# Optimization experiments

Hardware: AMD Instinct MI355X
Metric: run time of the kernel (lower is better)

Reference implementation:

```python
import jax, jax.numpy as jnp
import numpy as np

SEQ, BATCH, INPUT, HIDDEN, OUTPUT = 4096, 512, 8, 30, 1


def setup_inputs() -> dict:
    key = jax.random.key(0)
    ks = jax.random.split(key, 8)
    s = 1.0 / np.sqrt(HIDDEN)  # torch LSTM/Linear init scale
    u = lambda k, shape: jax.random.uniform(k, shape, jnp.float32, -s, s)
    return {
        "x": jax.random.normal(ks[0], (SEQ, BATCH, INPUT), jnp.float32),
        "W_ih": u(ks[1], (4 * HIDDEN, INPUT)),   # gate order: i, f, g, o
        "W_hh": u(ks[2], (4 * HIDDEN, HIDDEN)),
        "b_ih": u(ks[3], (4 * HIDDEN,)),
        "b_hh": u(ks[4], (4 * HIDDEN,)),
        "W_lin": u(ks[5], (OUTPUT, HIDDEN)),
        "b_lin": u(ks[6], (OUTPUT,)),
    }


def _lstm(x, W_ih, W_hh, b_ih, b_hh):
    H = W_hh.shape[1]
    B = x.shape[1]
    # Precompute input projections for all timesteps: [S,B,4H]
    x_proj = jnp.einsum("sbi,gi->sbg", x, W_ih) + b_ih + b_hh

    def step(carry, xp_t):
        h, c = carry
        gates = xp_t + h @ W_hh.T  # [B,4H]
        i, f, g, o = jnp.split(gates, 4, axis=-1)
        i, f, o = jax.nn.sigmoid(i), jax.nn.sigmoid(f), jax.nn.sigmoid(o)
        c = f * c + i * jnp.tanh(g)
        h = o * jnp.tanh(c)
        return (h, c), h

    h0 = jnp.zeros((B, H), x.dtype)
    c0 = jnp.zeros((B, H), x.dtype)
    _, pred = jax.lax.scan(step, (h0, c0), x_proj)
    return pred  # [S,B,H]


def reference(x, W_ih, W_hh, b_ih, b_hh, W_lin, b_lin):
    pred = _lstm(x, W_ih, W_hh, b_ih, b_hh)
    # per-timestep Linear (loop in the original == one batched matmul)
    out = jnp.einsum("sbh,oh->sbo", pred, W_lin) + b_lin
    return out
```

## Files before the change

kernel.cpp:

```cpp
#include <hip/hip_runtime.h>

#define SEQ 4096
#define BATCH 512
#define INP 8
#define HID 30
#define LOG2E 1.44269504088896340736f

typedef float f32x2 __attribute__((ext_vector_type(2)));
typedef float f32x4 __attribute__((ext_vector_type(4)));
typedef unsigned uint2v __attribute__((ext_vector_type(2)));

#define RCP(v)  __builtin_amdgcn_rcpf(v)
#if __has_builtin(__builtin_amdgcn_exp2f)
#define EXP2(v) __builtin_amdgcn_exp2f(v)
#else
#define EXP2(v) exp2f(v)
#endif
#define PKFMA(a, b, c) __builtin_elementwise_fma(a, b, c)

__device__ __forceinline__ f32x2 mk2(float a, float b) {
    f32x2 r; r.x = a; r.y = b; return r;
}

__device__ __forceinline__ void rep_halves(float v, float& lo_rep, float& hi_rep) {
#if __has_builtin(__builtin_amdgcn_permlane32_swap)
    uint2v r = __builtin_amdgcn_permlane32_swap(
        __float_as_uint(v), __float_as_uint(v), false, false);
    lo_rep = __uint_as_float(r.x);
    hi_rep = __uint_as_float(r.y);
#else
    float other = __shfl_xor(v, 32, 64);
    bool hi = (threadIdx.x & 32) != 0;
    lo_rep = hi ? other : v;
    hi_rep = hi ? v : other;
#endif
}

template <int CTRL>
__device__ __forceinline__ float dpp_sum_step(float v) {
    return v + __uint_as_float(__builtin_amdgcn_update_dpp(
        0, (int)__float_as_uint(v), CTRL, 0xf, 0xf, true));
}

__device__ __forceinline__ float group32_reduce(float v) {
    v = dpp_sum_step<0x111>(v);
    v = dpp_sum_step<0x112>(v);
    v = dpp_sum_step<0x114>(v);
    v = dpp_sum_step<0x118>(v);
#if __has_builtin(__builtin_amdgcn_permlane16_swap)
    uint2v r = __builtin_amdgcn_permlane16_swap(
        __float_as_uint(v), __float_as_uint(v), false, false);
    return __uint_as_float(r.x) + __uint_as_float(r.y);
#else
    return v + __shfl_xor(v, 16, 64);
#endif
}

__global__ __launch_bounds__(64)
__attribute__((amdgpu_waves_per_eu(1, 1)))
void lstm_chain_kernel(
    const float* __restrict__ x,
    const float* __restrict__ W_ih,
    const float* __restrict__ W_hh,
    const float* __restrict__ b_ih,
    const float* __restrict__ b_hh,
    const float* __restrict__ W_lin,
    const float* __restrict__ b_lin,
    float* __restrict__ out)
{
    const int lane = threadIdx.x;
    const int g    = blockIdx.x;
    const int b    = (g & 7) * (BATCH / 8) + (g >> 3);
    const int j    = lane & 31;
    const int half = lane >> 5;
    const int jc   = j < HID ? j : HID - 1;
    const int ra   = half * HID + jc;
    const int rb   = 2 * HID + half * HID + jc;

    const float sA   = -LOG2E;
    const float sB   = half ? -LOG2E : 2.0f * LOG2E;
    const float T2L  = 2.0f * LOG2E;
    const float IT2L = 1.0f / (2.0f * LOG2E);
    const float sclB2 = half ? T2L : -2.0f * T2L;
    const float addB2 = half ? 0.0f : T2L;

    f32x2 wih2_a[INP / 2], wih2_b[INP / 2];
#pragma unroll
    for (int i = 0; i < INP / 2; ++i) {
        f32x2 wa = mk2(W_ih[ra * INP + 2 * i] * sA, W_ih[ra * INP + 2 * i + 1] * sA);
        f32x2 wb = mk2(W_ih[rb * INP + 2 * i] * sB, W_ih[rb * INP + 2 * i + 1] * sB);
        asm volatile("" : "+v"(wa));
        asm volatile("" : "+v"(wb));
        wih2_a[i] = wa;
        wih2_b[i] = wb;
    }
    f32x2 whh2_a[HID / 2], whh2_b[HID / 2];
#pragma unroll
    for (int k = 0; k < HID / 2; ++k) {
        f32x2 wa = mk2(W_hh[ra * HID + 2 * k] * sA, W_hh[ra * HID + 2 * k + 1] * sA);
        f32x2 wb = mk2(W_hh[rb * HID + 2 * k] * sB, W_hh[rb * HID + 2 * k + 1] * sB);
        asm volatile("" : "+v"(wa));
        asm volatile("" : "+v"(wb));
        whh2_a[k] = wa;
        whh2_b[k] = wb;
    }
    const float bias_sa = (b_ih[ra] + b_hh[ra]) * sA;
    const float bias_sb = (b_ih[rb] + b_hh[rb]) * sB;
    const float blin    = b_lin[0];
    const float wlin    = (j < HID) ? W_lin[j] : 0.0f;

    __shared__ float s_y[SEQ];
    __shared__ __align__(16) float s_x[2 * 64 * INP];

    f32x4* sx4 = reinterpret_cast<f32x4*>(s_x);
    const f32x4* sx4c = reinterpret_cast<const f32x4*>(s_x);

    float hs[HID];
#pragma unroll
    for (int k = 0; k < HID; ++k) hs[k] = 0.0f;
    float c2 = 0.0f;

    f32x4 stg0, stg1;

#define STAGELOAD(CH2) do {                                                   \
    int _b0 = (CH2) * 64 + (lane >> 1);                                       \
    int _b1 = _b0 + 32;                                                       \
    if (_b0 > SEQ - 1) _b0 = SEQ - 1;                                         \
    if (_b1 > SEQ - 1) _b1 = SEQ - 1;                                         \
    const f32x4* _p0 = (const f32x4*)(x + ((size_t)_b0 * BATCH + b) * INP) + (lane & 1); \
    const f32x4* _p1 = (const f32x4*)(x + ((size_t)_b1 * BATCH + b) * INP) + (lane & 1); \
    stg0 = *_p0;                                                              \
    stg1 = *_p1;                                                              \
} while (0)

#define STAGEWRITE(CHW) do {                                                  \
    f32x4* _d = sx4 + ((CHW) & 1) * 128;                                      \
    _d[lane]      = stg0;                                                     \
    _d[64 + lane] = stg1;                                                     \
} while (0)

#define LOADXL(XA, XB, TL) do {                                               \
    int _e = (((TL) >> 6) & 1) * 128 + ((TL) & 63) * 2;                       \
    XA = sx4c[_e];                                                            \
    XB = sx4c[_e + 1];                                                        \
} while (0)

    f32x2 preA0, preA1, preB0, preB1;

#define IHPRE(XA, XB) do {                                                    \
    f32x2 x01 = __builtin_shufflevector(XA, XA, 0, 1);                        \
    f32x2 x23 = __builtin_shufflevector(XA, XA, 2, 3);                        \
    f32x2 x45 = __builtin_shufflevector(XB, XB, 0, 1);                        \
    f32x2 x67 = __builtin_shufflevector(XB, XB, 2, 3);                        \
    preA0 = mk2(bias_sa, 0.0f);  preB0 = mk2(bias_sb, 0.0f);                  \
    preA1 = mk2(0.0f, 0.0f);     preB1 = mk2(0.0f, 0.0f);                     \
    preA0 = PKFMA(x01, wih2_a[0], preA0);  preB0 = PKFMA(x01, wih2_b[0], preB0); \
    preA1 = PKFMA(x23, wih2_a[1], preA1);  preB1 = PKFMA(x23, wih2_b[1], preB1); \
    preA0 = PKFMA(x45, wih2_a[2], preA0);  preB0 = PKFMA(x45, wih2_b[2], preB0); \
    preA1 = PKFMA(x67, wih2_a[3], preA1);  preB1 = PKFMA(x67, wih2_b[3], preB1); \
} while (0)

    STAGELOAD(0);
    STAGEWRITE(0);
    STAGELOAD(1);

    f32x4 xA0, xB0, xA1, xB1, xA2, xB2, xA3, xB3;
    LOADXL(xA0, xB0, 0);  LOADXL(xA1, xB1, 1);
    LOADXL(xA2, xB2, 2);  LOADXL(xA3, xB3, 3);
    IHPRE(xA0, xB0);

#define STEP(T, XAn, XBn, XAl, XBl, TL) do {                                  \
    f32x2 A0 = preA0, A1 = preA1, B0 = preB0, B1 = preB1;                     \
    _Pragma("unroll")                                                         \
    for (int k = 0; k < HID / 2 - 1; k += 2) {                                \
        f32x2 h0 = mk2(hs[2*k],   hs[2*k+1]);                                 \
        f32x2 h1 = mk2(hs[2*k+2], hs[2*k+3]);                                 \
        A0 = PKFMA(h0, whh2_a[k],   A0);                                      \
        B0 = PKFMA(h0, whh2_b[k],   B0);                                      \
        A1 = PKFMA(h1, whh2_a[k+1], A1);                                      \
        B1 = PKFMA(h1, whh2_b[k+1], B1);                                      \
    }                                                                         \
    {                                                                         \
        f32x2 hT = mk2(hs[HID-2], hs[HID-1]);                                 \
        A0 = PKFMA(hT, whh2_a[HID/2-1], A0);                                  \
        B0 = PKFMA(hT, whh2_b[HID/2-1], B0);                                  \
    }                                                                         \
    f32x2 As = A0 + A1;  float ua = As.x + As.y;                              \
    f32x2 Bs = B0 + B1;  float ub = Bs.x + Bs.y;                              \
    float Av  = RCP(1.0f + EXP2(ua));              \
    float sBv = RCP(1.0f + EXP2(ub));                                         \
    float Bv2 = fmaf(sBv, sclB2, addB2);   \
               \
    float m = Av * (half ? c2 : Bv2);                                         \
    float mlo, mhi;                                                           \
    rep_halves(m, mlo, mhi);                                                  \
    c2 = mlo + mhi;                                   \
    float glo, oT2;                                                           \
    rep_halves(Bv2, glo, oT2);            \
    float oo_u = oT2 * IT2L;                                                  \
    float n2o  = oT2 * (-2.0f * IT2L);                                        \
    float sc = RCP(1.0f + EXP2(c2));                                          \
    float h  = fmaf(sc, n2o, oo_u);                        \
    _Pragma("unroll")                                                         \
    for (int k = 0; k < HID; ++k)                                             \
        hs[k] = __uint_as_float((unsigned)__builtin_amdgcn_readlane(          \
                    (int)__float_as_uint(h), k));                             \
                              \
    float p = group32_reduce(h * wlin);                                       \
    if (lane == 31) s_y[T] = p + blin;                                        \
    LOADXL(XAl, XBl, TL);                                                     \
    IHPRE(XAn, XBn);                                                          \
} while (0)

    for (int ch = 0; ch < SEQ / 64; ++ch) {
        STAGEWRITE(ch + 1);
        STAGELOAD(ch + 2);
        const int t0 = ch * 64;
#pragma unroll 1
        for (int tt = 0; tt < 64; tt += 4) {
            const int t = t0 + tt;
            STEP(t + 0, xA1, xB1, xA0, xB0, t + 4);
            STEP(t + 1, xA2, xB2, xA1, xB1, t + 5);
            STEP(t + 2, xA3, xB3, xA2, xB2, t + 6);
            STEP(t + 3, xA0, xB0, xA3, xB3, t + 7);
        }
    }
#undef STEP
#undef IHPRE
#undef LOADXL
#undef STAGELOAD
#undef STAGEWRITE

    __syncthreads();
    const float4* s_y4 = reinterpret_cast<const float4*>(s_y);
#pragma unroll 4
    for (int it = 0; it < SEQ / 256; ++it) {
        int tbase = it * 256 + lane * 4;
        float4 v = s_y4[tbase >> 2];
        out[(size_t)(tbase + 0) * BATCH + b] = v.x;
        out[(size_t)(tbase + 1) * BATCH + b] = v.y;
        out[(size_t)(tbase + 2) * BATCH + b] = v.z;
        out[(size_t)(tbase + 3) * BATCH + b] = v.w;
    }
}

extern "C" void kernel_launch(void* const* d_in, const int* in_sizes, int n_in,
                              void* d_out, int out_size, void* d_ws, size_t ws_size,
                              hipStream_t stream) {
    const float* x     = (const float*)d_in[0];
    const float* W_ih  = (const float*)d_in[1];
    const float* W_hh  = (const float*)d_in[2];
    const float* b_ih  = (const float*)d_in[3];
    const float* b_hh  = (const float*)d_in[4];
    const float* W_lin = (const float*)d_in[5];
    const float* b_lin = (const float*)d_in[6];
    float* out = (float*)d_out;

    lstm_chain_kernel<<<dim3(BATCH), dim3(64), 0, stream>>>(
        x, W_ih, W_hh, b_ih, b_hh, W_lin, b_lin, out);
}
```

Measured before the change: 1.020 ms.

## Process two batch chains per wave and broadcast h via LDS

Each 64-lane block now runs two independent LSTM batch chains, interleaved so their dependent FMA and transcendental sequences can hide each other's latency. The grid is halved to 256 blocks. The 30 per-step readlane broadcasts of h are replaced by one LDS store and vector LDS reads per chain. This trades half the grid's parallelism (fewer CUs busy on a 256-CU part) and more registers for better ILP within each wave. It also relies on LDS write-then-read ordering within a single wave, with no barrier.

```diff
diff --git a/kernel.cpp b/kernel.cpp
--- a/kernel.cpp
+++ b/kernel.cpp
@@ -70,7 +70,7 @@
 {
     const int lane = threadIdx.x;
     const int g    = blockIdx.x;
-    const int b    = (g & 7) * (BATCH / 8) + (g >> 3);
+    const int b0   = 2 * ((g & 7) * 32 + (g >> 3));
     const int j    = lane & 31;
     const int half = lane >> 5;
     const int jc   = j < HID ? j : HID - 1;
@@ -109,107 +109,175 @@
     const float blin    = b_lin[0];
     const float wlin    = (j < HID) ? W_lin[j] : 0.0f;
 
-    __shared__ float s_y[SEQ];
-    __shared__ __align__(16) float s_x[2 * 64 * INP];
+    __shared__ float s_y[2 * SEQ];
+    __shared__ __align__(16) float s_h[128];
+    __shared__ __align__(16) float s_x[2 * 2 * 64 * INP];
 
     f32x4* sx4 = reinterpret_cast<f32x4*>(s_x);
     const f32x4* sx4c = reinterpret_cast<const f32x4*>(s_x);
-
-    float hs[HID];
+    const f32x4* s_h4 = reinterpret_cast<const f32x4*>(s_h);
+
+    f32x2 hrf2P[HID / 2], hrf2Q[HID / 2];
 #pragma unroll
-    for (int k = 0; k < HID; ++k) hs[k] = 0.0f;
-    float c2 = 0.0f;
-
-    f32x4 stg0, stg1;
+    for (int k = 0; k < HID / 2; ++k) { hrf2P[k] = mk2(0.0f, 0.0f); hrf2Q[k] = mk2(0.0f, 0.0f); }
+    float c2P = 0.0f, c2Q = 0.0f;
+
+    f32x4 stg0, stg1, stg2, stg3;
 
 #define STAGELOAD(CH2) do {                                                   \
-    int _b0 = (CH2) * 64 + (lane >> 1);                                       \
-    int _b1 = _b0 + 32;                                                       \
-    if (_b0 > SEQ - 1) _b0 = SEQ - 1;                                         \
-    if (_b1 > SEQ - 1) _b1 = SEQ - 1;                                         \
-    const f32x4* _p0 = (const f32x4*)(x + ((size_t)_b0 * BATCH + b) * INP) + (lane & 1); \
-    const f32x4* _p1 = (const f32x4*)(x + ((size_t)_b1 * BATCH + b) * INP) + (lane & 1); \
-    stg0 = *_p0;                                                              \
-    stg1 = *_p1;                                                              \
+    int _s0 = (CH2) * 64 + (lane >> 1);                                       \
+    int _s1 = _s0 + 32;                                                       \
+    if (_s0 > SEQ - 1) _s0 = SEQ - 1;                                         \
+    if (_s1 > SEQ - 1) _s1 = SEQ - 1;                                         \
+    const f32x4* _pP0 = (const f32x4*)(x + ((size_t)_s0 * BATCH + b0) * INP) + (lane & 1);     \
+    const f32x4* _pP1 = (const f32x4*)(x + ((size_t)_s1 * BATCH + b0) * INP) + (lane & 1);     \
+    const f32x4* _pQ0 = (const f32x4*)(x + ((size_t)_s0 * BATCH + b0 + 1) * INP) + (lane & 1); \
+    const f32x4* _pQ1 = (const f32x4*)(x + ((size_t)_s1 * BATCH + b0 + 1) * INP) + (lane & 1); \
+    stg0 = *_pP0;  stg1 = *_pP1;  stg2 = *_pQ0;  stg3 = *_pQ1;                \
 } while (0)
 
 #define STAGEWRITE(CHW) do {                                                  \
-    f32x4* _d = sx4 + ((CHW) & 1) * 128;                                      \
-    _d[lane]      = stg0;                                                     \
-    _d[64 + lane] = stg1;                                                     \
-} while (0)
-
-#define LOADXL(XA, XB, TL) do {                                               \
-    int _e = (((TL) >> 6) & 1) * 128 + ((TL) & 63) * 2;                       \
-    XA = sx4c[_e];                                                            \
-    XB = sx4c[_e + 1];                                                        \
-} while (0)
-
-    f32x2 preA0, preA1, preB0, preB1;
-
-#define IHPRE(XA, XB) do {                                                    \
-    f32x2 x01 = __builtin_shufflevector(XA, XA, 0, 1);                        \
-    f32x2 x23 = __builtin_shufflevector(XA, XA, 2, 3);                        \
-    f32x2 x45 = __builtin_shufflevector(XB, XB, 0, 1);                        \
-    f32x2 x67 = __builtin_shufflevector(XB, XB, 2, 3);                        \
-    preA0 = mk2(bias_sa, 0.0f);  preB0 = mk2(bias_sb, 0.0f);                  \
-    preA1 = mk2(0.0f, 0.0f);     preB1 = mk2(0.0f, 0.0f);                     \
-    preA0 = PKFMA(x01, wih2_a[0], preA0);  preB0 = PKFMA(x01, wih2_b[0], preB0); \
-    preA1 = PKFMA(x23, wih2_a[1], preA1);  preB1 = PKFMA(x23, wih2_b[1], preB1); \
-    preA0 = PKFMA(x45, wih2_a[2], preA0);  preB0 = PKFMA(x45, wih2_b[2], preB0); \
-    preA1 = PKFMA(x67, wih2_a[3], preA1);  preB1 = PKFMA(x67, wih2_b[3], preB1); \
+    f32x4* _d = sx4 + ((CHW) & 1) * 256;                                      \
+    _d[lane]       = stg0;                                                    \
+    _d[64 + lane]  = stg1;                                                    \
+    _d[128 + lane] = stg2;                                                    \
+    _d[192 + lane] = stg3;                                                    \
+} while (0)
+
+#define LOADXL2(XAP, XBP, XAQ, XBQ, TL) do {                                  \
+    int _e = (((TL) >> 6) & 1) * 256 + ((TL) & 63) * 2;                       \
+    XAP = sx4c[_e];        XBP = sx4c[_e + 1];                                \
+    XAQ = sx4c[128 + _e];  XBQ = sx4c[128 + _e + 1];                          \
+} while (0)
+
+    f32x2 preA0P, preA1P, preB0P, preB1P;
+    f32x2 preA0Q, preA1Q, preB0Q, preB1Q;
+
+#define IHPRE2(XAP, XBP, XAQ, XBQ) do {                                       \
+    f32x2 p01 = __builtin_shufflevector(XAP, XAP, 0, 1);                      \
+    f32x2 q01 = __builtin_shufflevector(XAQ, XAQ, 0, 1);                      \
+    f32x2 p23 = __builtin_shufflevector(XAP, XAP, 2, 3);                      \
+    f32x2 q23 = __builtin_shufflevector(XAQ, XAQ, 2, 3);                      \
+    f32x2 p45 = __builtin_shufflevector(XBP, XBP, 0, 1);                      \
+    f32x2 q45 = __builtin_shufflevector(XBQ, XBQ, 0, 1);                      \
+    f32x2 p67 = __builtin_shufflevector(XBP, XBP, 2, 3);                      \
+    f32x2 q67 = __builtin_shufflevector(XBQ, XBQ, 2, 3);                      \
+    preA0P = PKFMA(p01, wih2_a[0], mk2(bias_sa, 0.0f));                       \
+    preA0Q = PKFMA(q01, wih2_a[0], mk2(bias_sa, 0.0f));                       \
+    preB0P = PKFMA(p01, wih2_b[0], mk2(bias_sb, 0.0f));                       \
+    preB0Q = PKFMA(q01, wih2_b[0], mk2(bias_sb, 0.0f));                       \
+    preA1P = PKFMA(p23, wih2_a[1], mk2(0.0f, 0.0f));                          \
+    preA1Q = PKFMA(q23, wih2_a[1], mk2(0.0f, 0.0f));                          \
+    preB1P = PKFMA(p23, wih2_b[1], mk2(0.0f, 0.0f));                          \
+    preB1Q = PKFMA(q23, wih2_b[1], mk2(0.0f, 0.0f));                          \
+    preA0P = PKFMA(p45, wih2_a[2], preA0P);                                   \
+    preA0Q = PKFMA(q45, wih2_a[2], preA0Q);                                   \
+    preB0P = PKFMA(p45, wih2_b[2], preB0P);                                   \
+    preB0Q = PKFMA(q45, wih2_b[2], preB0Q);                                   \
+    preA1P = PKFMA(p67, wih2_a[3], preA1P);                                   \
+    preA1Q = PKFMA(q67, wih2_a[3], preA1Q);                                   \
+    preB1P = PKFMA(p67, wih2_b[3], preB1P);                                   \
+    preB1Q = PKFMA(q67, wih2_b[3], preB1Q);                                   \
 } while (0)
 
     STAGELOAD(0);
     STAGEWRITE(0);
     STAGELOAD(1);
 
-    f32x4 xA0, xB0, xA1, xB1, xA2, xB2, xA3, xB3;
-    LOADXL(xA0, xB0, 0);  LOADXL(xA1, xB1, 1);
-    LOADXL(xA2, xB2, 2);  LOADXL(xA3, xB3, 3);
-    IHPRE(xA0, xB0);
-
-#define STEP(T, XAn, XBn, XAl, XBl, TL) do {                                  \
-    f32x2 A0 = preA0, A1 = preA1, B0 = preB0, B1 = preB1;                     \
+    f32x4 x0AP, x0BP, x0AQ, x0BQ;
+    f32x4 x1AP, x1BP, x1AQ, x1BQ;
+    LOADXL2(x0AP, x0BP, x0AQ, x0BQ, 0);
+    LOADXL2(x1AP, x1BP, x1AQ, x1BQ, 1);
+    IHPRE2(x0AP, x0BP, x0AQ, x0BQ);
+
+#define STEP2(T, nAP, nBP, nAQ, nBQ, lAP, lBP, lAQ, lBQ, TL) do {             \
+    f32x2 pA0 = preA0P, pA1 = preA1P, pB0 = preB0P, pB1 = preB1P;             \
+    f32x2 qA0 = preA0Q, qA1 = preA1Q, qB0 = preB0Q, qB1 = preB1Q;             \
     _Pragma("unroll")                                                         \
     for (int k = 0; k < HID / 2 - 1; k += 2) {                                \
-        f32x2 h0 = mk2(hs[2*k],   hs[2*k+1]);                                 \
-        f32x2 h1 = mk2(hs[2*k+2], hs[2*k+3]);                                 \
-        A0 = PKFMA(h0, whh2_a[k],   A0);                                      \
-        B0 = PKFMA(h0, whh2_b[k],   B0);                                      \
-        A1 = PKFMA(h1, whh2_a[k+1], A1);                                      \
-        B1 = PKFMA(h1, whh2_b[k+1], B1);                                      \
+        pA0 = PKFMA(hrf2P[k],   whh2_a[k],   pA0);                            \
+        qA0 = PKFMA(hrf2Q[k],   whh2_a[k],   qA0);                            \
+        pB0 = PKFMA(hrf2P[k],   whh2_b[k],   pB0);                            \
+        qB0 = PKFMA(hrf2Q[k],   whh2_b[k],   qB0);                            \
+        pA1 = PKFMA(hrf2P[k+1], whh2_a[k+1], pA1);                            \
+        qA1 = PKFMA(hrf2Q[k+1], whh2_a[k+1], qA1);                            \
+        pB1 = PKFMA(hrf2P[k+1], whh2_b[k+1], pB1);                            \
+        qB1 = PKFMA(hrf2Q[k+1], whh2_b[k+1], qB1);                            \
     }                                                                         \
-    {                                                                         \
-        f32x2 hT = mk2(hs[HID-2], hs[HID-1]);                                 \
-        A0 = PKFMA(hT, whh2_a[HID/2-1], A0);                                  \
-        B0 = PKFMA(hT, whh2_b[HID/2-1], B0);                                  \
-    }                                                                         \
-    f32x2 As = A0 + A1;  float ua = As.x + As.y;                              \
-    f32x2 Bs = B0 + B1;  float ub = Bs.x + Bs.y;                              \
-    float Av  = RCP(1.0f + EXP2(ua));              \
-    float sBv = RCP(1.0f + EXP2(ub));                                         \
-    float Bv2 = fmaf(sBv, sclB2, addB2);   \
-               \
-    float m = Av * (half ? c2 : Bv2);                                         \
-    float mlo, mhi;                                                           \
-    rep_halves(m, mlo, mhi);                                                  \
-    c2 = mlo + mhi;                                   \
-    float glo, oT2;                                                           \
-    rep_halves(Bv2, glo, oT2);            \
-    float oo_u = oT2 * IT2L;                                                  \
-    float n2o  = oT2 * (-2.0f * IT2L);                                        \
-    float sc = RCP(1.0f + EXP2(c2));                                          \
-    float h  = fmaf(sc, n2o, oo_u);                        \
-    _Pragma("unroll")                                                         \
-    for (int k = 0; k < HID; ++k)                                             \
-        hs[k] = __uint_as_float((unsigned)__builtin_amdgcn_readlane(          \
-                    (int)__float_as_uint(h), k));                             \
-                              \
-    float p = group32_reduce(h * wlin);                                       \
-    if (lane == 31) s_y[T] = p + blin;                                        \
-    LOADXL(XAl, XBl, TL);                                                     \
-    IHPRE(XAn, XBn);                                                          \
+    pA0 = PKFMA(hrf2P[HID/2-1], whh2_a[HID/2-1], pA0);                        \
+    qA0 = PKFMA(hrf2Q[HID/2-1], whh2_a[HID/2-1], qA0);                        \
+    pB0 = PKFMA(hrf2P[HID/2-1], whh2_b[HID/2-1], pB0);                        \
+    qB0 = PKFMA(hrf2Q[HID/2-1], whh2_b[HID/2-1], qB0);                        \
+    f32x2 AsP = pA0 + pA1;  f32x2 AsQ = qA0 + qA1;                            \
+    f32x2 BsP = pB0 + pB1;  f32x2 BsQ = qB0 + qB1;                            \
+    float uaP = AsP.x + AsP.y;  float uaQ = AsQ.x + AsQ.y;                    \
+    float ubP = BsP.x + BsP.y;  float ubQ = BsQ.x + BsQ.y;                    \
+    float AvP  = RCP(1.0f + EXP2(uaP));                                       \
+    float AvQ  = RCP(1.0f + EXP2(uaQ));                                       \
+    float sBvP = RCP(1.0f + EXP2(ubP));                                       \
+    float sBvQ = RCP(1.0f + EXP2(ubQ));                                       \
+    float BvP2 = fmaf(sBvP, sclB2, addB2);                                    \
+    float BvQ2 = fmaf(sBvQ, sclB2, addB2);                                    \
+                  \
+    float mP = AvP * (half ? c2P : BvP2);                                     \
+    float mQ = AvQ * (half ? c2Q : BvQ2);                                     \
+    float mloP, mhiP, mloQ, mhiQ;                                             \
+    rep_halves(mP, mloP, mhiP);                                               \
+    rep_halves(mQ, mloQ, mhiQ);                                               \
+    c2P = mloP + mhiP;                                                        \
+    c2Q = mloQ + mhiQ;                                                        \
+    float gloP, oT2P, gloQ, oT2Q;                                             \
+    rep_halves(BvP2, gloP, oT2P);                                             \
+    rep_halves(BvQ2, gloQ, oT2Q);                                             \
+    float oo_uP = oT2P * IT2L;           float oo_uQ = oT2Q * IT2L;           \
+    float n2oP  = oT2P * (-2.0f * IT2L); float n2oQ  = oT2Q * (-2.0f * IT2L); \
+    float scP = RCP(1.0f + EXP2(c2P));                                        \
+    float scQ = RCP(1.0f + EXP2(c2Q));                                        \
+    float hP  = fmaf(scP, n2oP, oo_uP);                                       \
+    float hQ  = fmaf(scQ, n2oQ, oo_uQ);                                       \
+    s_h[lane]      = hP;                                                      \
+    s_h[64 + lane] = hQ;                                                      \
+    f32x4 hvP0 = s_h4[0],  hvP1 = s_h4[1],  hvP2 = s_h4[2],  hvP3 = s_h4[3];  \
+    f32x4 hvP4 = s_h4[4],  hvP5 = s_h4[5],  hvP6 = s_h4[6],  hvP7 = s_h4[7];  \
+    f32x4 hvQ0 = s_h4[16], hvQ1 = s_h4[17], hvQ2 = s_h4[18], hvQ3 = s_h4[19]; \
+    f32x4 hvQ4 = s_h4[20], hvQ5 = s_h4[21], hvQ6 = s_h4[22], hvQ7 = s_h4[23]; \
+                                 \
+    float pP = group32_reduce(hP * wlin);                                     \
+    float pQ = group32_reduce(hQ * wlin);                                     \
+    if (lane == 31) { s_y[T] = pP + blin;  s_y[SEQ + (T)] = pQ + blin; }      \
+    LOADXL2(lAP, lBP, lAQ, lBQ, TL);                                          \
+    IHPRE2(nAP, nBP, nAQ, nBQ);                                               \
+                                             \
+    hrf2P[0]  = __builtin_shufflevector(hvP0, hvP0, 0, 1);                    \
+    hrf2P[1]  = __builtin_shufflevector(hvP0, hvP0, 2, 3);                    \
+    hrf2P[2]  = __builtin_shufflevector(hvP1, hvP1, 0, 1);                    \
+    hrf2P[3]  = __builtin_shufflevector(hvP1, hvP1, 2, 3);                    \
+    hrf2P[4]  = __builtin_shufflevector(hvP2, hvP2, 0, 1);                    \
+    hrf2P[5]  = __builtin_shufflevector(hvP2, hvP2, 2, 3);                    \
+    hrf2P[6]  = __builtin_shufflevector(hvP3, hvP3, 0, 1);                    \
+    hrf2P[7]  = __builtin_shufflevector(hvP3, hvP3, 2, 3);                    \
+    hrf2P[8]  = __builtin_shufflevector(hvP4, hvP4, 0, 1);                    \
+    hrf2P[9]  = __builtin_shufflevector(hvP4, hvP4, 2, 3);                    \
+    hrf2P[10] = __builtin_shufflevector(hvP5, hvP5, 0, 1);                    \
+    hrf2P[11] = __builtin_shufflevector(hvP5, hvP5, 2, 3);                    \
+    hrf2P[12] = __builtin_shufflevector(hvP6, hvP6, 0, 1);                    \
+    hrf2P[13] = __builtin_shufflevector(hvP6, hvP6, 2, 3);                    \
+    hrf2P[14] = __builtin_shufflevector(hvP7, hvP7, 0, 1);                    \
+    hrf2Q[0]  = __builtin_shufflevector(hvQ0, hvQ0, 0, 1);                    \
+    hrf2Q[1]  = __builtin_shufflevector(hvQ0, hvQ0, 2, 3);                    \
+    hrf2Q[2]  = __builtin_shufflevector(hvQ1, hvQ1, 0, 1);                    \
+    hrf2Q[3]  = __builtin_shufflevector(hvQ1, hvQ1, 2, 3);                    \
+    hrf2Q[4]  = __builtin_shufflevector(hvQ2, hvQ2, 0, 1);                    \
+    hrf2Q[5]  = __builtin_shufflevector(hvQ2, hvQ2, 2, 3);                    \
+    hrf2Q[6]  = __builtin_shufflevector(hvQ3, hvQ3, 0, 1);                    \
+    hrf2Q[7]  = __builtin_shufflevector(hvQ3, hvQ3, 2, 3);                    \
+    hrf2Q[8]  = __builtin_shufflevector(hvQ4, hvQ4, 0, 1);                    \
+    hrf2Q[9]  = __builtin_shufflevector(hvQ4, hvQ4, 2, 3);                    \
+    hrf2Q[10] = __builtin_shufflevector(hvQ5, hvQ5, 0, 1);                    \
+    hrf2Q[11] = __builtin_shufflevector(hvQ5, hvQ5, 2, 3);                    \
+    hrf2Q[12] = __builtin_shufflevector(hvQ6, hvQ6, 0, 1);                    \
+    hrf2Q[13] = __builtin_shufflevector(hvQ6, hvQ6, 2, 3);                    \
+    hrf2Q[14] = __builtin_shufflevector(hvQ7, hvQ7, 0, 1);                    \
 } while (0)
 
     for (int ch = 0; ch < SEQ / 64; ++ch) {
@@ -217,30 +285,31 @@
         STAGELOAD(ch + 2);
         const int t0 = ch * 64;
 #pragma unroll 1
-        for (int tt = 0; tt < 64; tt += 4) {
+        for (int tt = 0; tt < 64; tt += 2) {
             const int t = t0 + tt;
-            STEP(t + 0, xA1, xB1, xA0, xB0, t + 4);
-            STEP(t + 1, xA2, xB2, xA1, xB1, t + 5);
-            STEP(t + 2, xA3, xB3, xA2, xB2, t + 6);
-            STEP(t + 3, xA0, xB0, xA3, xB3, t + 7);
+            STEP2(t,     x1AP, x1BP, x1AQ, x1BQ, x0AP, x0BP, x0AQ, x0BQ, t + 2);
+            STEP2(t + 1, x0AP, x0BP, x0AQ, x0BQ, x1AP, x1BP, x1AQ, x1BQ, t + 3);
         }
     }
-#undef STEP
-#undef IHPRE
-#undef LOADXL
+#undef STEP2
+#undef IHPRE2
+#undef LOADXL2
 #undef STAGELOAD
 #undef STAGEWRITE
 
     __syncthreads();
     const float4* s_y4 = reinterpret_cast<const float4*>(s_y);
+#pragma unroll 2
+    for (int c = 0; c < 2; ++c) {
 #pragma unroll 4
-    for (int it = 0; it < SEQ / 256; ++it) {
-        int tbase = it * 256 + lane * 4;
-        float4 v = s_y4[tbase >> 2];
-        out[(size_t)(tbase + 0) * BATCH + b] = v.x;
-        out[(size_t)(tbase + 1) * BATCH + b] = v.y;
-        out[(size_t)(tbase + 2) * BATCH + b] = v.z;
-        out[(size_t)(tbase + 3) * BATCH + b] = v.w;
+        for (int it = 0; it < SEQ / 256; ++it) {
+            int tbase = it * 256 + lane * 4;
+            float4 v = s_y4[(c * SEQ + tbase) >> 2];
+            out[(size_t)(tbase + 0) * BATCH + b0 + c] = v.x;
+            out[(size_t)(tbase + 1) * BATCH + b0 + c] = v.y;
+            out[(size_t)(tbase + 2) * BATCH + b0 + c] = v.z;
+            out[(size_t)(tbase + 3) * BATCH + b0 + c] = v.w;
+        }
     }
 }
 
@@ -256,6 +325,6 @@
     const float* b_lin = (const float*)d_in[6];
     float* out = (float*)d_out;
 
-    lstm_chain_kernel<<<dim3(BATCH), dim3(64), 0, stream>>>(
+    lstm_chain_kernel<<<dim3(BATCH / 2), dim3(64), 0, stream>>>(
         x, W_ih, W_hh, b_ih, b_hh, W_lin, b_lin, out);
 }
```

After: 1.668 ms. +63.5%, slower.
